# Optimization experiments

Hardware: AMD Instinct MI355X
Metric: run time of the kernel (lower is better)

The kernel has to match this reference:

```python
import jax, jax.numpy as jnp
import numpy as np

B, L, C = 64, 64, 16          # batch, seq_len, chars per word
V, CV = 100000, 100           # word vocab, char vocab
EMB, CHD = 300, 64            # word emb dim, char emb dim
N_HIGHWAY, N_ATTN = 2, 2
D = EMB + 3 * 50              # highway_dim = 450


def setup_inputs() -> dict:
    ks = jax.random.split(jax.random.key(0), 16)
    word_emb = jax.random.normal(ks[6], (V, EMB), jnp.float32) * 0.01
    word_emb = word_emb.at[0].set(0.0)  # padding_idx row zeroed
    return {
        "q1": jax.random.randint(ks[0], (B, L), 0, V),
        "q2": jax.random.randint(ks[1], (B, L), 0, V),
        "q1_len": jax.random.randint(ks[2], (B,), 1, L + 1),
        "q2_len": jax.random.randint(ks[3], (B,), 1, L + 1),
        "q1_char": jax.random.randint(ks[4], (B, L, C), 0, CV),
        "q2_char": jax.random.randint(ks[5], (B, L, C), 0, CV),
        "word_emb": word_emb,
        "char_emb": jax.random.normal(ks[7], (CV, CHD), jnp.float32) * 0.1,
        "conv_w3": jax.random.normal(ks[8], (50, CHD, 3), jnp.float32) / np.sqrt(CHD * 3),
        "conv_b3": jnp.zeros((50,), jnp.float32),
        "conv_w4": jax.random.normal(ks[9], (50, CHD, 4), jnp.float32) / np.sqrt(CHD * 4),
        "conv_b4": jnp.zeros((50,), jnp.float32),
        "conv_w5": jax.random.normal(ks[10], (50, CHD, 5), jnp.float32) / np.sqrt(CHD * 5),
        "conv_b5": jnp.zeros((50,), jnp.float32),
        "hw_w": jax.random.normal(ks[11], (D, D), jnp.float32) / np.sqrt(D),
        "hw_b": jnp.zeros((D,), jnp.float32),
        "attn_w": jax.random.normal(ks[12], (N_ATTN, 3 * D), jnp.float32) / np.sqrt(3 * D),
        "attn_b": jnp.zeros((N_ATTN,), jnp.float32),
    }


def _char_features(qc, emb, convs):
    # qc: [B, T, C] int -> [B, T, 150]
    Bq, T, Cc = qc.shape
    e = emb[qc.reshape(-1, Cc)].transpose(0, 2, 1)  # [B*T, CHD, C]
    outs = []
    for w, b in convs:
        h = jax.lax.conv_general_dilated(e, w, (1,), 'VALID',
                                         dimension_numbers=('NCH', 'OIH', 'NCH'))
        h = jax.nn.relu(h + b[None, :, None])
        outs.append(jnp.max(h, axis=2))  # max over char positions
    return jnp.concatenate(outs, axis=-1).reshape(Bq, T, -1)


def _highway(x, w, b):
    # NB: original reuses the SAME linear for transform and gate (bug-faithful)
    y = x @ w.T + b
    g = jax.nn.sigmoid(y)
    return g * jax.nn.relu(y) + (1.0 - g) * x


def _self_attn(x, mask, w, b):
    # Exact decomposition of Linear(concat(x_i, x_j, x_i*x_j)) -> scalar:
    # score[b,i,j] = x_i.w1 + x_j.w2 + sum_d x_i x_j w3 + b
    d = x.shape[-1]
    w1, w2, w3 = w[:d], w[d:2 * d], w[2 * d:]
    scores = ((x @ w1)[:, :, None] + (x @ w2)[:, None, :]
              + jnp.einsum('bid,bjd->bij', x * w3, x) + b)
    # original masked_fill uses -1e-09 (not -1e9) -- reproduce faithfully
    logits = jnp.where(mask[:, None, :], scores, jnp.float32(-1e-9))
    attn = jax.nn.softmax(logits, axis=-1)
    return jnp.einsum('bij,bjd->bid', attn, x)


def _branch(q, q_char, q_len, word_emb, char_emb, convs, hw_w, hw_b, attn_w, attn_b):
    mask = jnp.arange(L)[None, :] < q_len[:, None]
    x = jnp.concatenate([word_emb[q], _char_features(q_char, char_emb, convs)], axis=-1)
    for _ in range(N_HIGHWAY):
        x = _highway(x, hw_w, hw_b)
    att = x
    for i in range(N_ATTN):
        att = _self_attn(x, mask, attn_w[i], attn_b[i])
        x = att + x
    return att


def reference(q1, q2, q1_len, q2_len, q1_char, q2_char, word_emb, char_emb,
              conv_w3, conv_b3, conv_w4, conv_b4, conv_w5, conv_b5,
              hw_w, hw_b, attn_w, attn_b):
    convs = [(conv_w3, conv_b3), (conv_w4, conv_b4), (conv_w5, conv_b5)]
    a1 = _branch(q1, q1_char, q1_len, word_emb, char_emb, convs, hw_w, hw_b, attn_w, attn_b)
    a2 = _branch(q2, q2_char, q2_len, word_emb, char_emb, convs, hw_w, hw_b, attn_w, attn_b)
    return (a1, a2)
```

## Files before the change

### kernel.cpp

```cpp
#include <hip/hip_runtime.h>
#include <math.h>

#define B   64
#define L   64
#define C   16
#define CHD 64
#define EMB 300
#define D   450
#define DP  480
#define NT  (B*L)
#define NBH 128

typedef short bf16x8 __attribute__((ext_vector_type(8)));
typedef float f32x4  __attribute__((ext_vector_type(4)));
typedef float f32x2  __attribute__((ext_vector_type(2)));
typedef unsigned short ushort_t;
typedef ushort_t us4 __attribute__((ext_vector_type(4)));

#define MFMA16 __builtin_amdgcn_mfma_f32_16x16x32_bf16

#define WPF_N (10 * 10 * 512)
#define WBF_N (32 * 15 * 512)
#define XFRAG 30720

#define XFS 456
#define XSS 488

__device__ inline float wave_sum(float v) {
#pragma unroll
    for (int o = 32; o; o >>= 1) v += __shfl_xor(v, o, 64);
    return v;
}
__device__ inline ushort_t f2b(float f) {
    union { float f; unsigned u; } c; c.f = f;
    unsigned r = c.u + 0x7FFFu + ((c.u >> 16) & 1u);
    return (ushort_t)(r >> 16);
}

__global__ __launch_bounds__(256) void prep_kernel(
    const float* __restrict__ W,
    const float* __restrict__ w3, const float* __restrict__ b3,
    const float* __restrict__ w4, const float* __restrict__ b4,
    const float* __restrict__ w5, const float* __restrict__ b5,
    const float* __restrict__ char_emb,
    ushort_t* __restrict__ Wb16F, ushort_t* __restrict__ WpadF,
    float* __restrict__ bias160, ushort_t* __restrict__ ceb16)
{
    int idx = blockIdx.x * 256 + threadIdx.x;
    if (idx < WBF_N) {
        const int e = idx & 7, l = (idx >> 3) & 63, t = idx >> 9;
        const int ks = t % 15, nt = t / 15;
        const int ln = l & 15, q = l >> 4;
        const int n = nt * 16 + ln, k = ks * 32 + q * 8 + e;
        float v = (n < D && k < D) ? W[(size_t)n * D + k] : 0.f;
        Wb16F[idx] = f2b(v);
        return;
    }
    idx -= WBF_N;
    if (idx < WPF_N) {
        const int e = idx & 7, l = (idx >> 3) & 63, t = idx >> 9;
        const int ks = t % 10, nt = t / 10;
        const int ln = l & 15, q = l >> 4;
        const int f = nt * 16 + ln;
        const int kd = ks * 32 + q * 8 + e;
        const int k = kd >> 6, d = kd & 63;
        float v = 0.f;
        if (f < 50)       { if (k < 3) v = w3[f * 192 + d * 3 + k]; }
        else if (f < 100) { if (k < 4) v = w4[(f - 50) * 256 + d * 4 + k]; }
        else if (f < 150) { v = w5[(f - 100) * 320 + d * 5 + k]; }
        WpadF[idx] = f2b(v);
        return;
    }
    idx -= WPF_N;
    if (idx < 160) {
        bias160[idx] = (idx < 50) ? b3[idx] : (idx < 100) ? b4[idx - 50]
                     : (idx < 150) ? b5[idx - 100] : 0.f;
    } else if (idx < 160 + 100 * 64) {
        int i = idx - 160;
        ceb16[i] = f2b(char_emb[i]);
    }
}

#define ESS 72
#define EST (20 * ESS)

__global__ __launch_bounds__(256) void embed_conv_kernel(
    const int* __restrict__ q1, const int* __restrict__ q2,
    const int* __restrict__ q1c, const int* __restrict__ q2c,
    const float* __restrict__ word_emb, const ushort_t* __restrict__ ceb16,
    const ushort_t* __restrict__ WpadF, const float* __restrict__ bias160,
    float* __restrict__ xout, ushort_t* __restrict__ xbF)
{
    __shared__ ushort_t es[8 * EST];
    __shared__ ushort_t Xt[8 * XSS];

    const int tid  = threadIdx.x;
    const int wv   = tid >> 6;
    const int lane = tid & 63;
    const int ln   = lane & 15, quad = lane >> 4;
    const int bx   = blockIdx.x;
    const int tokbase = ((bx & 7) * 128 + (bx >> 3)) * 8;

#pragma unroll
    for (int i = 0; i < 4; ++i) {
        int c = tid + i * 256;
        int row = c >> 3, part = c & 7;
        int tl = row >> 4, cr = row & 15;
        int gtok   = tokbase + tl;
        int branch = gtok >> 12;
        int tokl   = gtok & (NT - 1);
        int cid    = (branch ? q2c : q1c)[tokl * C + cr];
        *(bf16x8*)&es[tl * EST + cr * ESS + part * 8] =
            *(const bf16x8*)&ceb16[cid * 64 + part * 8];
    }
    {
        int tl = tid >> 5, rr = (tid >> 3) & 3, part = tid & 7;
        bf16x8 z = {0, 0, 0, 0, 0, 0, 0, 0};
        *(bf16x8*)&es[tl * EST + (16 + rr) * ESS + part * 8] = z;
    }

#pragma unroll 1
    for (int c = tid; c < 8 * 75; c += 256) {
        const int t  = c / 75, d4 = c - t * 75;
        const int tok    = tokbase + t;
        const int branch = tok >> 12;
        const int tokl   = tok & (NT - 1);
        const int w      = (branch ? q2 : q1)[tokl];
        const float4 v = *(const float4*)(word_emb + (size_t)w * EMB + d4 * 4);
        float* dst = xout + (size_t)tok * D + d4 * 4;
        *(f32x2*)dst       = (f32x2){v.x, v.y};
        *(f32x2*)(dst + 2) = (f32x2){v.z, v.w};
        us4 pk = { f2b(v.x), f2b(v.y), f2b(v.z), f2b(v.w) };
        *(us4*)&Xt[t * XSS + d4 * 4] = pk;
    }
    if (tid < 240) {
        const int t = tid / 30, k = tid - t * 30;
        Xt[t * XSS + D + k] = 0;
    }
    __syncthreads();

    const int t0 = wv * 2, t1 = t0 + 1;
    f32x4 acc[2][10];
#pragma unroll
    for (int t = 0; t < 2; ++t)
#pragma unroll
        for (int nt = 0; nt < 10; ++nt) acc[t][nt] = (f32x4){0.f, 0.f, 0.f, 0.f};

#pragma unroll 1
    for (int ks = 0; ks < 10; ++ks) {
        const int kk   = ks * 32 + quad * 8;
        const int arow = kk >> 6, aoff = kk & 63;
        bf16x8 a0 = *(const bf16x8*)&es[t0 * EST + (ln + arow) * ESS + aoff];
        bf16x8 a1 = *(const bf16x8*)&es[t1 * EST + (ln + arow) * ESS + aoff];
#pragma unroll
        for (int nt = 0; nt < 10; ++nt) {
            bf16x8 bf = *(const bf16x8*)&WpadF[(size_t)((nt * 10 + ks) << 9) + lane * 8];
            acc[0][nt] = MFMA16(a0, bf, acc[0][nt], 0, 0, 0);
            acc[1][nt] = MFMA16(a1, bf, acc[1][nt], 0, 0, 0);
        }
    }
    __syncthreads();

    float* smf = (float*)es;
#pragma unroll
    for (int t = 0; t < 2; ++t) {
        const int tloc = t0 + t;
#pragma unroll
        for (int nt = 0; nt < 10; ++nt) {
            const int f  = nt * 16 + ln;
            const int Pf = (f < 50) ? 14 : (f < 100) ? 13 : 12;
            float m = -1e30f;
#pragma unroll
            for (int r = 0; r < 4; ++r) {
                const int p = quad * 4 + r;
                if (p < Pf) m = fmaxf(m, acc[t][nt][r]);
            }
            m = fmaxf(m, __shfl_xor(m, 16, 64));
            m = fmaxf(m, __shfl_xor(m, 32, 64));
            if (quad == 0) smf[tloc * 160 + f] = fmaxf(0.f, m + bias160[f]);
        }
    }
    __syncthreads();
#pragma unroll 1
    for (int c = tid; c < 8 * 150; c += 256) {
        const int t = c / 150, f = c - t * 150;
        const float rv = smf[t * 160 + f];
        xout[(size_t)(tokbase + t) * D + EMB + f] = rv;
        Xt[t * XSS + EMB + f] = f2b(rv);
    }
    __syncthreads();

    {
        const int tile = tokbase >> 4, half = (tokbase >> 3) & 1;
#pragma unroll 1
        for (int c = tid; c < 480; c += 256) {
            const int ksl = c >> 5, s = c & 31;
            const int q = s >> 3, tl = s & 7;
            const int l = q * 16 + half * 8 + tl;
            bf16x8 v = *(const bf16x8*)&Xt[tl * XSS + ksl * 32 + q * 8];
            *(bf16x8*)&xbF[((size_t)(tile * 15 + ksl) * 64 + l) * 8] = v;
        }
    }
}

#define HLS 72

__global__ __launch_bounds__(256, 4) void highway_mfma_kernel(
    const ushort_t* __restrict__ xbFi, const float* __restrict__ xf32,
    const ushort_t* __restrict__ Wb16F, const float* __restrict__ bvec,
    float* __restrict__ out, ushort_t* __restrict__ xbFo)
{
    __shared__ ushort_t Xl[64 * HLS];

    const int bx = blockIdx.x;
    const int cx = bx & 7, rr = bx >> 3;
    const int my = cx * 16 + (rr & 15);
    const int mx = rr >> 4;

    const int tid  = threadIdx.x;
    const int wv   = tid >> 6;
    const int lane = tid & 63;
    const int wm = wv >> 1, wn = wv & 1;
    const int m0 = my * 64 + wm * 32;
    const int n0 = mx * 64 + wn * 32;
    const int lm = lane & 15, quad = lane >> 4;

    const int tA0 = my * 4 + wm * 2;
    const ushort_t* ax0 = xbFi + (size_t)(tA0 * 15) * 512 + lane * 8;
    const ushort_t* ax1 = ax0 + 15 * 512;
    const int ntg0 = mx * 4 + wn * 2;
    const ushort_t* bw0 = Wb16F + (size_t)(ntg0 * 15) * 512 + lane * 8;
    const ushort_t* bw1 = bw0 + 15 * 512;

    f32x4 acc[2][2];
#pragma unroll
    for (int i = 0; i < 2; ++i)
#pragma unroll
        for (int j = 0; j < 2; ++j) acc[i][j] = (f32x4){0.f, 0.f, 0.f, 0.f};

#pragma unroll 3
    for (int ks = 0; ks < 15; ++ks) {
        bf16x8 a0 = *(const bf16x8*)(ax0 + ks * 512);
        bf16x8 a1 = *(const bf16x8*)(ax1 + ks * 512);
        bf16x8 b0 = *(const bf16x8*)(bw0 + ks * 512);
        bf16x8 b1 = *(const bf16x8*)(bw1 + ks * 512);
        acc[0][0] = MFMA16(a0, b0, acc[0][0], 0, 0, 0);
        acc[0][1] = MFMA16(a0, b1, acc[0][1], 0, 0, 0);
        acc[1][0] = MFMA16(a1, b0, acc[1][0], 0, 0, 0);
        acc[1][1] = MFMA16(a1, b1, acc[1][1], 0, 0, 0);
    }

#pragma unroll
    for (int nt = 0; nt < 2; ++nt) {
        const int n  = n0 + nt * 16 + lm;
        const int nl = wn * 32 + nt * 16 + lm;
        const bool nval = (n < D);
        const float bv = nval ? bvec[n] : 0.f;
#pragma unroll
        for (int mt = 0; mt < 2; ++mt) {
#pragma unroll
            for (int r = 0; r < 4; ++r) {
                const int m  = m0 + mt * 16 + quad * 4 + r;
                const int ml = wm * 32 + mt * 16 + quad * 4 + r;
                float y = acc[mt][nt][r] + bv;
                float g = 1.f / (1.f + __expf(-y));
                float o = 0.f;
                if (nval) {
                    float xo = xf32[(size_t)m * D + n];
                    o = g * fmaxf(y, 0.f) + (1.f - g) * xo;
                    out[(size_t)m * D + n] = o;
                }
                Xl[ml * HLS + nl] = f2b(nval ? o : 0.f);
            }
        }
    }
    __syncthreads();

#pragma unroll 1
    for (int c = tid; c < 512; c += 256) {
        const int fi = c >> 6, l = c & 63;
        const int tl = fi >> 1, ksl = fi & 1;
        const int ksg = mx * 2 + ksl;
        if (ksg < 15) {
            const int lnp = l & 15, qp = l >> 4;
            bf16x8 v = *(const bf16x8*)&Xl[(tl * 16 + lnp) * HLS + ksl * 32 + qp * 8];
            *(bf16x8*)&xbFo[((size_t)((my * 4 + tl) * 15 + ksg) * 64 + l) * 8] = v;
        }
    }
}

__global__ __launch_bounds__(512, 4) void highway2_prep_kernel(
    const ushort_t* __restrict__ xbFi, const float* __restrict__ xf32in,
    const ushort_t* __restrict__ Wb16F, const float* __restrict__ bvec,
    const float* __restrict__ attn_w,
    float* __restrict__ outf, ushort_t* __restrict__ xbFo,
    ushort_t* __restrict__ xw3F, ushort_t* __restrict__ xTF,
    float* __restrict__ s1g, float* __restrict__ s2g)
{
    __shared__ float Xf[16 * XFS];

    const int bx  = blockIdx.x;
    const int wid = (bx & 7) * 64 + (bx >> 3);
    const int bh  = wid >> 2, jq = wid & 3;
    const int tt  = wid;
    const int m0  = tt * 16;
    const int tid = threadIdx.x;
    const int wv  = tid >> 6;
    const int lane = tid & 63;
    const int ln = lane & 15, quad = lane >> 4;

    const ushort_t* ax = xbFi + (size_t)(tt * 15) * 512 + lane * 8;
    f32x4 acc[4];
#pragma unroll
    for (int t = 0; t < 4; ++t) acc[t] = (f32x4){0.f, 0.f, 0.f, 0.f};

#pragma unroll 1
    for (int ks = 0; ks < 15; ++ks) {
        bf16x8 a = *(const bf16x8*)(ax + ks * 512);
#pragma unroll
        for (int t = 0; t < 4; ++t) {
            const int nt = wv * 4 + t;
            if (nt < 30) {
                bf16x8 b = *(const bf16x8*)&Wb16F[(size_t)(nt * 15 + ks) * 512 + lane * 8];
                acc[t] = MFMA16(a, b, acc[t], 0, 0, 0);
            }
        }
    }

#pragma unroll
    for (int t = 0; t < 4; ++t) {
        const int nt = wv * 4 + t;
        if (nt >= 30) continue;
        const int n = nt * 16 + ln;
        const bool nval = (n < D);
        const float bv = nval ? bvec[n] : 0.f;
#pragma unroll
        for (int reg = 0; reg < 4; ++reg) {
            const int i = quad * 4 + reg;
            float y = acc[t][reg] + bv;
            float g = 1.f / (1.f + __expf(-y));
            if (nval) {
                float xo = xf32in[(size_t)(m0 + i) * D + n];
                float o = g * fmaxf(y, 0.f) + (1.f - g) * xo;
                outf[(size_t)(m0 + i) * D + n] = o;
                Xf[i * XFS + n] = o;
            }
        }
    }
    __syncthreads();

    const float* wb = attn_w;
    const float* w3 = wb + 2 * D;

#pragma unroll 1
    for (int rr = 0; rr < 2; ++rr) {
        const int j = wv * 2 + rr;
        float a1 = 0.f, a2 = 0.f;
#pragma unroll
        for (int t = 0; t < 8; ++t) {
            const int k = lane + t * 64;
            if (k < D) {
                float xv = Xf[j * XFS + k];
                a1 = fmaf(xv, wb[k], a1);
                a2 = fmaf(xv, wb[D + k], a2);
            }
        }
        a1 = wave_sum(a1);
        a2 = wave_sum(a2);
        if (lane == 0) { s1g[m0 + j] = a1; s2g[m0 + j] = a2; }
    }

#pragma unroll 1
    for (int c = tid; c < 960; c += 512) {
        const int ks = c >> 6, l = c & 63;
        const int lnp = l & 15, qp = l >> 4;
        bf16x8 v, pv;
#pragma unroll
        for (int e = 0; e < 8; ++e) {
            const int k = ks * 32 + qp * 8 + e;
            const float x = (k < D) ? Xf[lnp * XFS + k] : 0.f;
            v[e]  = (short)((k < D) ? f2b(x) : 0);
            pv[e] = (short)f2b((k < D) ? x * w3[k] : 0.f);
        }
        *(bf16x8*)&xbFo[((size_t)(tt * 15 + ks) * 64 + l) * 8] = v;
        *(bf16x8*)&xw3F[(size_t)bh * XFRAG + ((jq * 15 + ks) * 64 + l) * 8] = pv;
    }

    {
        const int half = jq >> 1, q0 = (jq & 1) * 2;
#pragma unroll 1
        for (int c = tid; c < 960; c += 512) {
            const int dt = c >> 5, s = c & 31;
            const int qp = q0 + (s >> 4), lnp = s & 15;
            const int d  = dt * 16 + lnp;
            const int jb = (qp & 1) * 8;
            bf16x8 v;
#pragma unroll
            for (int e = 0; e < 8; ++e)
                v[e] = (short)((d < D) ? f2b(Xf[(jb + e) * XFS + d]) : 0);
            *(bf16x8*)&xTF[(size_t)bh * XFRAG + ((dt * 2 + half) * 64 + qp * 16 + lnp) * 8] = v;
        }
    }
}

#define ALS 72

__global__ __launch_bounds__(512, 4) void attn_core_prep_kernel(
    const float* __restrict__ xf32,
    const ushort_t* __restrict__ xF, const ushort_t* __restrict__ xw3F,
    const ushort_t* __restrict__ xTF,
    const float* __restrict__ s1g, const float* __restrict__ s2g,
    const int* __restrict__ q1_len, const int* __restrict__ q2_len,
    const float* __restrict__ attn_b, const float* __restrict__ attn_w,
    ushort_t* __restrict__ xbFo,
    ushort_t* __restrict__ xw3Fo, ushort_t* __restrict__ xTFo,
    float* __restrict__ s1o, float* __restrict__ s2o)
{
    __shared__ float    sc[16][68];
    __shared__ ushort_t Al[16 * ALS];
    __shared__ float    Qp[4 * 256];
    __shared__ float    Af[16 * XFS];

    const int bx  = blockIdx.x;
    const int wid = (bx & 7) * 64 + (bx >> 3);
    const int bh  = wid >> 2, iq = wid & 3;
    const int branch = bh >> 6, b = bh & 63;
    const int tid  = threadIdx.x;
    const int wv   = tid >> 6;
    const int lane = tid & 63;
    const int ln   = lane & 15, quad = lane >> 4;
    const int i0   = iq * 16;
    const int m0   = bh * 64 + i0;
    const int jt   = wv & 3, hks = wv >> 2;

    const ushort_t* xa = xF   + (size_t)bh * XFRAG + (iq * 15 * 64 + lane) * 8;
    const ushort_t* xb = xw3F + (size_t)bh * XFRAG + (jt * 15 * 64 + lane) * 8;

    f32x4 qa = (f32x4){0.f, 0.f, 0.f, 0.f};
    if (hks == 0) {
#pragma unroll
        for (int ks = 0; ks < 15; ks += 2) {
            bf16x8 a  = *(const bf16x8*)(xa + ks * 512);
            bf16x8 bq = *(const bf16x8*)(xb + ks * 512);
            qa = MFMA16(a, bq, qa, 0, 0, 0);
        }
    } else {
#pragma unroll
        for (int ks = 1; ks < 15; ks += 2) {
            bf16x8 a  = *(const bf16x8*)(xa + ks * 512);
            bf16x8 bq = *(const bf16x8*)(xb + ks * 512);
            qa = MFMA16(a, bq, qa, 0, 0, 0);
        }
        *(f32x4*)&Qp[jt * 256 + lane * 4] = qa;
    }
    __syncthreads();

    const int   len  = (branch ? q2_len : q1_len)[b];
    if (hks == 0) {
        f32x4 qo = *(const f32x4*)&Qp[jt * 256 + lane * 4];
        f32x4 qacc = qa + qo;
        const float bias = attn_b[0];
        const int   j    = jt * 16 + ln;
        const float s2v  = s2g[bh * 64 + j];
#pragma unroll
        for (int reg = 0; reg < 4; ++reg) {
            const int i = i0 + quad * 4 + reg;
            float v = qacc[reg] + s1g[bh * 64 + i] + s2v + bias;
            if (j >= len) v = -1e-9f;
            sc[quad * 4 + reg][j] = v;
        }
    }
    __syncthreads();

#pragma unroll
    for (int rr = 0; rr < 2; ++rr) {
        const int r = wv * 2 + rr;
        float v = sc[r][lane];
        float m = v;
#pragma unroll
        for (int o = 32; o; o >>= 1) m = fmaxf(m, __shfl_xor(m, o, 64));
        float ev = __expf(v - m);
        float sm = ev;
#pragma unroll
        for (int o = 32; o; o >>= 1) sm += __shfl_xor(sm, o, 64);
        Al[r * ALS + lane] = f2b(ev * (1.f / sm));
    }
    __syncthreads();

    const ushort_t* xTb = xTF + (size_t)bh * XFRAG + lane * 8;
    bf16x8 af0 = *(const bf16x8*)&Al[ln * ALS + quad * 8];
    bf16x8 af1 = *(const bf16x8*)&Al[ln * ALS + quad * 8 + 32];

#pragma unroll 2
    for (int dt = wv; dt < 30; dt += 8) {
        bf16x8 b0 = *(const bf16x8*)(xTb + dt * 1024);
        bf16x8 b1 = *(const bf16x8*)(xTb + dt * 1024 + 512);
        f32x4 acc = (f32x4){0.f, 0.f, 0.f, 0.f};
        acc = MFMA16(af0, b0, acc, 0, 0, 0);
        acc = MFMA16(af1, b1, acc, 0, 0, 0);

        const int d = dt * 16 + ln;
        if (d < D) {
#pragma unroll
            for (int reg = 0; reg < 4; ++reg) {
                const int il = quad * 4 + reg;
                float v = acc[reg] + xf32[(size_t)(m0 + il) * D + d];
                Af[il * XFS + d] = v;
            }
        }
    }
    __syncthreads();

    const float* wb1 = attn_w + 3 * D;
    const float* w31 = wb1 + 2 * D;

#pragma unroll 1
    for (int rr = 0; rr < 2; ++rr) {
        const int jj = wv * 2 + rr;
        float a1 = 0.f, a2 = 0.f;
#pragma unroll
        for (int t = 0; t < 8; ++t) {
            const int k = lane + t * 64;
            if (k < D) {
                float xv = Af[jj * XFS + k];
                a1 = fmaf(xv, wb1[k], a1);
                a2 = fmaf(xv, wb1[D + k], a2);
            }
        }
        a1 = wave_sum(a1);
        a2 = wave_sum(a2);
        if (lane == 0) { s1o[m0 + jj] = a1; s2o[m0 + jj] = a2; }
    }

#pragma unroll 1
    for (int c = tid; c < 960; c += 512) {
        const int ks = c >> 6, l = c & 63;
        const int lnp = l & 15, qp = l >> 4;
        bf16x8 v, pv;
#pragma unroll
        for (int e = 0; e < 8; ++e) {
            const int k = ks * 32 + qp * 8 + e;
            const float x = (k < D) ? Af[lnp * XFS + k] : 0.f;
            v[e]  = (short)((k < D) ? f2b(x) : 0);
            pv[e] = (short)f2b((k < D) ? x * w31[k] : 0.f);
        }
        *(bf16x8*)&xbFo[((size_t)((bh * 4 + iq) * 15 + ks) * 64 + l) * 8] = v;
        *(bf16x8*)&xw3Fo[(size_t)bh * XFRAG + ((iq * 15 + ks) * 64 + l) * 8] = pv;
    }

    {
        const int half = iq >> 1, q0 = (iq & 1) * 2;
#pragma unroll 1
        for (int c = tid; c < 960; c += 512) {
            const int dt = c >> 5, s = c & 31;
            const int qp = q0 + (s >> 4), lnp = s & 15;
            const int d  = dt * 16 + lnp;
            const int jb = (qp & 1) * 8;
            bf16x8 v;
#pragma unroll
            for (int e = 0; e < 8; ++e)
                v[e] = (short)((d < D) ? f2b(Af[(jb + e) * XFS + d]) : 0);
            *(bf16x8*)&xTFo[(size_t)bh * XFRAG + ((dt * 2 + half) * 64 + qp * 16 + lnp) * 8] = v;
        }
    }
}

__global__ __launch_bounds__(512, 4) void attn_core_final_kernel(
    const ushort_t* __restrict__ xF, const ushort_t* __restrict__ xw3F,
    const ushort_t* __restrict__ xTF,
    const float* __restrict__ s1g, const float* __restrict__ s2g,
    const int* __restrict__ q1_len, const int* __restrict__ q2_len,
    const float* __restrict__ attn_b,
    float* __restrict__ outf)
{
    __shared__ float    sc[16][68];
    __shared__ ushort_t Al[16 * ALS];
    __shared__ float    Qp[4 * 256];

    const int bx  = blockIdx.x;
    const int wid = (bx & 7) * 64 + (bx >> 3);
    const int bh  = wid >> 2, iq = wid & 3;
    const int branch = bh >> 6, b = bh & 63;
    const int tid  = threadIdx.x;
    const int wv   = tid >> 6;
    const int lane = tid & 63;
    const int ln   = lane & 15, quad = lane >> 4;
    const int i0   = iq * 16;
    const int jt   = wv & 3, hks = wv >> 2;

    const ushort_t* xa = xF   + (size_t)bh * XFRAG + (iq * 15 * 64 + lane) * 8;
    const ushort_t* xb = xw3F + (size_t)bh * XFRAG + (jt * 15 * 64 + lane) * 8;

    f32x4 qa = (f32x4){0.f, 0.f, 0.f, 0.f};
    if (hks == 0) {
#pragma unroll
        for (int ks = 0; ks < 15; ks += 2) {
            bf16x8 a  = *(const bf16x8*)(xa + ks * 512);
            bf16x8 bq = *(const bf16x8*)(xb + ks * 512);
            qa = MFMA16(a, bq, qa, 0, 0, 0);
        }
    } else {
#pragma unroll
        for (int ks = 1; ks < 15; ks += 2) {
            bf16x8 a  = *(const bf16x8*)(xa + ks * 512);
            bf16x8 bq = *(const bf16x8*)(xb + ks * 512);
            qa = MFMA16(a, bq, qa, 0, 0, 0);
        }
        *(f32x4*)&Qp[jt * 256 + lane * 4] = qa;
    }
    __syncthreads();

    const int len = (branch ? q2_len : q1_len)[b];
    if (hks == 0) {
        f32x4 qo = *(const f32x4*)&Qp[jt * 256 + lane * 4];
        f32x4 qacc = qa + qo;
        const float bias = attn_b[1];
        const int   j    = jt * 16 + ln;
        const float s2v  = s2g[bh * 64 + j];
#pragma unroll
        for (int reg = 0; reg < 4; ++reg) {
            const int i = i0 + quad * 4 + reg;
            float v = qacc[reg] + s1g[bh * 64 + i] + s2v + bias;
            if (j >= len) v = -1e-9f;
            sc[quad * 4 + reg][j] = v;
        }
    }
    __syncthreads();

#pragma unroll
    for (int rr = 0; rr < 2; ++rr) {
        const int r = wv * 2 + rr;
        float v = sc[r][lane];
        float m = v;
#pragma unroll
        for (int o = 32; o; o >>= 1) m = fmaxf(m, __shfl_xor(m, o, 64));
        float ev = __expf(v - m);
        float sm = ev;
#pragma unroll
        for (int o = 32; o; o >>= 1) sm += __shfl_xor(sm, o, 64);
        Al[r * ALS + lane] = f2b(ev * (1.f / sm));
    }
    __syncthreads();

    const ushort_t* xTb = xTF + (size_t)bh * XFRAG + lane * 8;
    bf16x8 af0 = *(const bf16x8*)&Al[ln * ALS + quad * 8];
    bf16x8 af1 = *(const bf16x8*)&Al[ln * ALS + quad * 8 + 32];

#pragma unroll 2
    for (int dt = wv; dt < 30; dt += 8) {
        bf16x8 b0 = *(const bf16x8*)(xTb + dt * 1024);
        bf16x8 b1 = *(const bf16x8*)(xTb + dt * 1024 + 512);
        f32x4 acc = (f32x4){0.f, 0.f, 0.f, 0.f};
        acc = MFMA16(af0, b0, acc, 0, 0, 0);
        acc = MFMA16(af1, b1, acc, 0, 0, 0);

        const int d = dt * 16 + ln;
        if (d < D) {
#pragma unroll
            for (int reg = 0; reg < 4; ++reg) {
                const int i = i0 + quad * 4 + reg;
                outf[((size_t)bh * 64 + i) * D + d] = acc[reg];
            }
        }
    }
}

extern "C" void kernel_launch(void* const* d_in, const int* in_sizes, int n_in,
                              void* d_out, int out_size, void* d_ws, size_t ws_size,
                              hipStream_t stream) {
    const int*   q1       = (const int*)  d_in[0];
    const int*   q2       = (const int*)  d_in[1];
    const int*   q1_len   = (const int*)  d_in[2];
    const int*   q2_len   = (const int*)  d_in[3];
    const int*   q1c      = (const int*)  d_in[4];
    const int*   q2c      = (const int*)  d_in[5];
    const float* word_emb = (const float*)d_in[6];
    const float* char_emb = (const float*)d_in[7];
    const float* w3       = (const float*)d_in[8];
    const float* b3       = (const float*)d_in[9];
    const float* w4       = (const float*)d_in[10];
    const float* b4       = (const float*)d_in[11];
    const float* w5       = (const float*)d_in[12];
    const float* b5       = (const float*)d_in[13];
    const float* hw_w     = (const float*)d_in[14];
    const float* hw_b     = (const float*)d_in[15];
    const float* attn_w   = (const float*)d_in[16];
    const float* attn_b   = (const float*)d_in[17];
    float* out = (float*)d_out;

    float*    buf0    = (float*)d_ws;
    float*    buf1    = buf0 + (size_t)2 * NT * D;
    float*    bias160 = buf1 + (size_t)2 * NT * D;
    ushort_t* xbFa    = (ushort_t*)(bias160 + 160);
    ushort_t* xbFb    = xbFa + (size_t)2 * NT * DP;
    ushort_t* Wb16F   = xbFb + (size_t)2 * NT * DP;
    ushort_t* WpadF   = Wb16F + (size_t)WBF_N;
    ushort_t* ceb16   = WpadF + (size_t)WPF_N;
    ushort_t* xw3Fa   = ceb16 + (size_t)100 * 64;
    ushort_t* xTFa    = xw3Fa + (size_t)NBH * XFRAG;
    ushort_t* xw3Fb   = xTFa  + (size_t)NBH * XFRAG;
    ushort_t* xTFb    = xw3Fb + (size_t)NBH * XFRAG;
    float*    s1a     = (float*)(xTFb + (size_t)NBH * XFRAG);
    float*    s2a     = s1a + (size_t)2 * NT;
    float*    s1b     = s2a + (size_t)2 * NT;
    float*    s2b     = s1b + (size_t)2 * NT;

    prep_kernel<<<(WBF_N + WPF_N + 160 + 100 * 64 + 255) / 256, 256, 0, stream>>>(
        hw_w, w3, b3, w4, b4, w5, b5, char_emb, Wb16F, WpadF, bias160, ceb16);
    embed_conv_kernel<<<1024, 256, 0, stream>>>(q1, q2, q1c, q2c, word_emb, ceb16,
                                                WpadF, bias160, buf0, xbFa);

    highway_mfma_kernel<<<1024, 256, 0, stream>>>(xbFa, buf0, Wb16F, hw_b, buf1, xbFb);

    highway2_prep_kernel<<<512, 512, 0, stream>>>(
        xbFb, buf1, Wb16F, hw_b, attn_w, buf0, xbFa, xw3Fa, xTFa, s1a, s2a);

    attn_core_prep_kernel<<<512, 512, 0, stream>>>(
        buf0, xbFa, xw3Fa, xTFa, s1a, s2a, q1_len, q2_len, attn_b, attn_w,
        xbFb, xw3Fb, xTFb, s1b, s2b);

    attn_core_final_kernel<<<512, 512, 0, stream>>>(
        xbFb, xw3Fb, xTFb, s1b, s2b, q1_len, q2_len, attn_b, out);
}
```

Measured before the change: 306.0 us.

## Fuse embedding, char conv and both highway layers into one front kernel

Merges the embed+char-conv kernel, the first highway kernel and the second highway/attention-prep kernel into a single megafront kernel. Each block handles 16 tokens and keeps the activations in fp32 shared memory across stages, converting to bf16 on the fly for the MFMA A operand. This removes two launches and the global round-trips of intermediate fp32 and bf16-fragment buffers. The cost is that each block now streams the whole highway weight matrix twice, with scalar LDS reads and conversions to build A fragments, and uses more shared memory, which may lower occupancy.

```diff
diff --git a/kernel.cpp b/kernel.cpp
--- a/kernel.cpp
+++ b/kernel.cpp
@@ -13,9 +13,7 @@
 
 typedef short bf16x8 __attribute__((ext_vector_type(8)));
 typedef float f32x4  __attribute__((ext_vector_type(4)));
-typedef float f32x2  __attribute__((ext_vector_type(2)));
 typedef unsigned short ushort_t;
-typedef ushort_t us4 __attribute__((ext_vector_type(4)));
 
 #define MFMA16 __builtin_amdgcn_mfma_f32_16x16x32_bf16
 
@@ -23,8 +21,7 @@
 #define WBF_N (32 * 15 * 512)
 #define XFRAG 30720
 
-#define XFS 456
-#define XSS 488
+#define XFS 457
 
 __device__ inline float wave_sum(float v) {
 #pragma unroll
@@ -84,220 +81,19 @@
 #define ESS 72
 #define EST (20 * ESS)
 
-__global__ __launch_bounds__(256) void embed_conv_kernel(
+__global__ __launch_bounds__(512, 4) void megafront_kernel(
     const int* __restrict__ q1, const int* __restrict__ q2,
     const int* __restrict__ q1c, const int* __restrict__ q2c,
     const float* __restrict__ word_emb, const ushort_t* __restrict__ ceb16,
     const ushort_t* __restrict__ WpadF, const float* __restrict__ bias160,
-    float* __restrict__ xout, ushort_t* __restrict__ xbF)
-{
-    __shared__ ushort_t es[8 * EST];
-    __shared__ ushort_t Xt[8 * XSS];
-
-    const int tid  = threadIdx.x;
-    const int wv   = tid >> 6;
-    const int lane = tid & 63;
-    const int ln   = lane & 15, quad = lane >> 4;
-    const int bx   = blockIdx.x;
-    const int tokbase = ((bx & 7) * 128 + (bx >> 3)) * 8;
-
-#pragma unroll
-    for (int i = 0; i < 4; ++i) {
-        int c = tid + i * 256;
-        int row = c >> 3, part = c & 7;
-        int tl = row >> 4, cr = row & 15;
-        int gtok   = tokbase + tl;
-        int branch = gtok >> 12;
-        int tokl   = gtok & (NT - 1);
-        int cid    = (branch ? q2c : q1c)[tokl * C + cr];
-        *(bf16x8*)&es[tl * EST + cr * ESS + part * 8] =
-            *(const bf16x8*)&ceb16[cid * 64 + part * 8];
-    }
-    {
-        int tl = tid >> 5, rr = (tid >> 3) & 3, part = tid & 7;
-        bf16x8 z = {0, 0, 0, 0, 0, 0, 0, 0};
-        *(bf16x8*)&es[tl * EST + (16 + rr) * ESS + part * 8] = z;
-    }
-
-#pragma unroll 1
-    for (int c = tid; c < 8 * 75; c += 256) {
-        const int t  = c / 75, d4 = c - t * 75;
-        const int tok    = tokbase + t;
-        const int branch = tok >> 12;
-        const int tokl   = tok & (NT - 1);
-        const int w      = (branch ? q2 : q1)[tokl];
-        const float4 v = *(const float4*)(word_emb + (size_t)w * EMB + d4 * 4);
-        float* dst = xout + (size_t)tok * D + d4 * 4;
-        *(f32x2*)dst       = (f32x2){v.x, v.y};
-        *(f32x2*)(dst + 2) = (f32x2){v.z, v.w};
-        us4 pk = { f2b(v.x), f2b(v.y), f2b(v.z), f2b(v.w) };
-        *(us4*)&Xt[t * XSS + d4 * 4] = pk;
-    }
-    if (tid < 240) {
-        const int t = tid / 30, k = tid - t * 30;
-        Xt[t * XSS + D + k] = 0;
-    }
-    __syncthreads();
-
-    const int t0 = wv * 2, t1 = t0 + 1;
-    f32x4 acc[2][10];
-#pragma unroll
-    for (int t = 0; t < 2; ++t)
-#pragma unroll
-        for (int nt = 0; nt < 10; ++nt) acc[t][nt] = (f32x4){0.f, 0.f, 0.f, 0.f};
-
-#pragma unroll 1
-    for (int ks = 0; ks < 10; ++ks) {
-        const int kk   = ks * 32 + quad * 8;
-        const int arow = kk >> 6, aoff = kk & 63;
-        bf16x8 a0 = *(const bf16x8*)&es[t0 * EST + (ln + arow) * ESS + aoff];
-        bf16x8 a1 = *(const bf16x8*)&es[t1 * EST + (ln + arow) * ESS + aoff];
-#pragma unroll
-        for (int nt = 0; nt < 10; ++nt) {
-            bf16x8 bf = *(const bf16x8*)&WpadF[(size_t)((nt * 10 + ks) << 9) + lane * 8];
-            acc[0][nt] = MFMA16(a0, bf, acc[0][nt], 0, 0, 0);
-            acc[1][nt] = MFMA16(a1, bf, acc[1][nt], 0, 0, 0);
-        }
-    }
-    __syncthreads();
-
-    float* smf = (float*)es;
-#pragma unroll
-    for (int t = 0; t < 2; ++t) {
-        const int tloc = t0 + t;
-#pragma unroll
-        for (int nt = 0; nt < 10; ++nt) {
-            const int f  = nt * 16 + ln;
-            const int Pf = (f < 50) ? 14 : (f < 100) ? 13 : 12;
-            float m = -1e30f;
-#pragma unroll
-            for (int r = 0; r < 4; ++r) {
-                const int p = quad * 4 + r;
-                if (p < Pf) m = fmaxf(m, acc[t][nt][r]);
-            }
-            m = fmaxf(m, __shfl_xor(m, 16, 64));
-            m = fmaxf(m, __shfl_xor(m, 32, 64));
-            if (quad == 0) smf[tloc * 160 + f] = fmaxf(0.f, m + bias160[f]);
-        }
-    }
-    __syncthreads();
-#pragma unroll 1
-    for (int c = tid; c < 8 * 150; c += 256) {
-        const int t = c / 150, f = c - t * 150;
-        const float rv = smf[t * 160 + f];
-        xout[(size_t)(tokbase + t) * D + EMB + f] = rv;
-        Xt[t * XSS + EMB + f] = f2b(rv);
-    }
-    __syncthreads();
-
-    {
-        const int tile = tokbase >> 4, half = (tokbase >> 3) & 1;
-#pragma unroll 1
-        for (int c = tid; c < 480; c += 256) {
-            const int ksl = c >> 5, s = c & 31;
-            const int q = s >> 3, tl = s & 7;
-            const int l = q * 16 + half * 8 + tl;
-            bf16x8 v = *(const bf16x8*)&Xt[tl * XSS + ksl * 32 + q * 8];
-            *(bf16x8*)&xbF[((size_t)(tile * 15 + ksl) * 64 + l) * 8] = v;
-        }
-    }
-}
-
-#define HLS 72
-
-__global__ __launch_bounds__(256, 4) void highway_mfma_kernel(
-    const ushort_t* __restrict__ xbFi, const float* __restrict__ xf32,
-    const ushort_t* __restrict__ Wb16F, const float* __restrict__ bvec,
-    float* __restrict__ out, ushort_t* __restrict__ xbFo)
-{
-    __shared__ ushort_t Xl[64 * HLS];
-
-    const int bx = blockIdx.x;
-    const int cx = bx & 7, rr = bx >> 3;
-    const int my = cx * 16 + (rr & 15);
-    const int mx = rr >> 4;
-
-    const int tid  = threadIdx.x;
-    const int wv   = tid >> 6;
-    const int lane = tid & 63;
-    const int wm = wv >> 1, wn = wv & 1;
-    const int m0 = my * 64 + wm * 32;
-    const int n0 = mx * 64 + wn * 32;
-    const int lm = lane & 15, quad = lane >> 4;
-
-    const int tA0 = my * 4 + wm * 2;
-    const ushort_t* ax0 = xbFi + (size_t)(tA0 * 15) * 512 + lane * 8;
-    const ushort_t* ax1 = ax0 + 15 * 512;
-    const int ntg0 = mx * 4 + wn * 2;
-    const ushort_t* bw0 = Wb16F + (size_t)(ntg0 * 15) * 512 + lane * 8;
-    const ushort_t* bw1 = bw0 + 15 * 512;
-
-    f32x4 acc[2][2];
-#pragma unroll
-    for (int i = 0; i < 2; ++i)
-#pragma unroll
-        for (int j = 0; j < 2; ++j) acc[i][j] = (f32x4){0.f, 0.f, 0.f, 0.f};
-
-#pragma unroll 3
-    for (int ks = 0; ks < 15; ++ks) {
-        bf16x8 a0 = *(const bf16x8*)(ax0 + ks * 512);
-        bf16x8 a1 = *(const bf16x8*)(ax1 + ks * 512);
-        bf16x8 b0 = *(const bf16x8*)(bw0 + ks * 512);
-        bf16x8 b1 = *(const bf16x8*)(bw1 + ks * 512);
-        acc[0][0] = MFMA16(a0, b0, acc[0][0], 0, 0, 0);
-        acc[0][1] = MFMA16(a0, b1, acc[0][1], 0, 0, 0);
-        acc[1][0] = MFMA16(a1, b0, acc[1][0], 0, 0, 0);
-        acc[1][1] = MFMA16(a1, b1, acc[1][1], 0, 0, 0);
-    }
-
-#pragma unroll
-    for (int nt = 0; nt < 2; ++nt) {
-        const int n  = n0 + nt * 16 + lm;
-        const int nl = wn * 32 + nt * 16 + lm;
-        const bool nval = (n < D);
-        const float bv = nval ? bvec[n] : 0.f;
-#pragma unroll
-        for (int mt = 0; mt < 2; ++mt) {
-#pragma unroll
-            for (int r = 0; r < 4; ++r) {
-                const int m  = m0 + mt * 16 + quad * 4 + r;
-                const int ml = wm * 32 + mt * 16 + quad * 4 + r;
-                float y = acc[mt][nt][r] + bv;
-                float g = 1.f / (1.f + __expf(-y));
-                float o = 0.f;
-                if (nval) {
-                    float xo = xf32[(size_t)m * D + n];
-                    o = g * fmaxf(y, 0.f) + (1.f - g) * xo;
-                    out[(size_t)m * D + n] = o;
-                }
-                Xl[ml * HLS + nl] = f2b(nval ? o : 0.f);
-            }
-        }
-    }
-    __syncthreads();
-
-#pragma unroll 1
-    for (int c = tid; c < 512; c += 256) {
-        const int fi = c >> 6, l = c & 63;
-        const int tl = fi >> 1, ksl = fi & 1;
-        const int ksg = mx * 2 + ksl;
-        if (ksg < 15) {
-            const int lnp = l & 15, qp = l >> 4;
-            bf16x8 v = *(const bf16x8*)&Xl[(tl * 16 + lnp) * HLS + ksl * 32 + qp * 8];
-            *(bf16x8*)&xbFo[((size_t)((my * 4 + tl) * 15 + ksg) * 64 + l) * 8] = v;
-        }
-    }
-}
-
-__global__ __launch_bounds__(512, 4) void highway2_prep_kernel(
-    const ushort_t* __restrict__ xbFi, const float* __restrict__ xf32in,
-    const ushort_t* __restrict__ Wb16F, const float* __restrict__ bvec,
+    const ushort_t* __restrict__ Wb16F, const float* __restrict__ hw_b,
     const float* __restrict__ attn_w,
     float* __restrict__ outf, ushort_t* __restrict__ xbFo,
     ushort_t* __restrict__ xw3F, ushort_t* __restrict__ xTF,
     float* __restrict__ s1g, float* __restrict__ s2g)
 {
-    __shared__ float Xf[16 * XFS];
+    __shared__ ushort_t es[16 * EST];
+    __shared__ float    Xf[16 * XFS];
 
     const int bx  = blockIdx.x;
     const int wid = (bx & 7) * 64 + (bx >> 3);
@@ -309,45 +105,134 @@
     const int lane = tid & 63;
     const int ln = lane & 15, quad = lane >> 4;
 
-    const ushort_t* ax = xbFi + (size_t)(tt * 15) * 512 + lane * 8;
-    f32x4 acc[4];
-#pragma unroll
-    for (int t = 0; t < 4; ++t) acc[t] = (f32x4){0.f, 0.f, 0.f, 0.f};
-
-#pragma unroll 1
-    for (int ks = 0; ks < 15; ++ks) {
-        bf16x8 a = *(const bf16x8*)(ax + ks * 512);
+#pragma unroll
+    for (int i = 0; i < 4; ++i) {
+        int c = tid + i * 512;
+        int row = c >> 3, part = c & 7;
+        int tl = row >> 4, cr = row & 15;
+        int gtok   = m0 + tl;
+        int branch = gtok >> 12;
+        int tokl   = gtok & (NT - 1);
+        int cid    = (branch ? q2c : q1c)[tokl * C + cr];
+        *(bf16x8*)&es[tl * EST + cr * ESS + part * 8] =
+            *(const bf16x8*)&ceb16[cid * 64 + part * 8];
+    }
+    {
+        int tl = tid >> 5, rr = (tid >> 3) & 3, part = tid & 7;
+        bf16x8 z = {0, 0, 0, 0, 0, 0, 0, 0};
+        *(bf16x8*)&es[tl * EST + (16 + rr) * ESS + part * 8] = z;
+    }
+
+#pragma unroll 1
+    for (int c = tid; c < 16 * 75; c += 512) {
+        const int t  = c / 75, d4 = c - t * 75;
+        const int gtok   = m0 + t;
+        const int branch = gtok >> 12;
+        const int tokl   = gtok & (NT - 1);
+        const int w      = (branch ? q2 : q1)[tokl];
+        const float4 v = *(const float4*)(word_emb + (size_t)w * EMB + d4 * 4);
+        float* dst = &Xf[t * XFS + d4 * 4];
+        dst[0] = v.x; dst[1] = v.y; dst[2] = v.z; dst[3] = v.w;
+    }
+    __syncthreads();
+
+    {
+        const int t0 = wv * 2, t1 = t0 + 1;
+        f32x4 acc[2][10];
+#pragma unroll
+        for (int t = 0; t < 2; ++t)
+#pragma unroll
+            for (int nt = 0; nt < 10; ++nt) acc[t][nt] = (f32x4){0.f, 0.f, 0.f, 0.f};
+
+#pragma unroll 1
+        for (int ks = 0; ks < 10; ++ks) {
+            const int kk   = ks * 32 + quad * 8;
+            const int arow = kk >> 6, aoff = kk & 63;
+            bf16x8 a0 = *(const bf16x8*)&es[t0 * EST + (ln + arow) * ESS + aoff];
+            bf16x8 a1 = *(const bf16x8*)&es[t1 * EST + (ln + arow) * ESS + aoff];
+#pragma unroll
+            for (int nt = 0; nt < 10; ++nt) {
+                bf16x8 bf = *(const bf16x8*)&WpadF[(size_t)((nt * 10 + ks) << 9) + lane * 8];
+                acc[0][nt] = MFMA16(a0, bf, acc[0][nt], 0, 0, 0);
+                acc[1][nt] = MFMA16(a1, bf, acc[1][nt], 0, 0, 0);
+            }
+        }
+        __syncthreads();
+
+        float* smf = (float*)es;
+#pragma unroll
+        for (int t = 0; t < 2; ++t) {
+            const int tloc = t0 + t;
+#pragma unroll
+            for (int nt = 0; nt < 10; ++nt) {
+                const int f  = nt * 16 + ln;
+                const int Pf = (f < 50) ? 14 : (f < 100) ? 13 : 12;
+                float m = -1e30f;
+#pragma unroll
+                for (int r = 0; r < 4; ++r) {
+                    const int p = quad * 4 + r;
+                    if (p < Pf) m = fmaxf(m, acc[t][nt][r]);
+                }
+                m = fmaxf(m, __shfl_xor(m, 16, 64));
+                m = fmaxf(m, __shfl_xor(m, 32, 64));
+                if (quad == 0) smf[tloc * 160 + f] = fmaxf(0.f, m + bias160[f]);
+            }
+        }
+        __syncthreads();
+#pragma unroll 1
+        for (int c = tid; c < 16 * 150; c += 512) {
+            const int t = c / 150, f = c - t * 150;
+            Xf[t * XFS + EMB + f] = smf[t * 160 + f];
+        }
+    }
+    __syncthreads();
+
+#pragma unroll 1
+    for (int h = 0; h < 2; ++h) {
+        f32x4 hacc[4];
+#pragma unroll
+        for (int t = 0; t < 4; ++t) hacc[t] = (f32x4){0.f, 0.f, 0.f, 0.f};
+
+#pragma unroll 1
+        for (int ks = 0; ks < 15; ++ks) {
+            bf16x8 a;
+#pragma unroll
+            for (int e = 0; e < 8; ++e) {
+                const int k = ks * 32 + quad * 8 + e;
+                a[e] = (short)((k < D) ? f2b(Xf[ln * XFS + k]) : 0);
+            }
+#pragma unroll
+            for (int t = 0; t < 4; ++t) {
+                const int nt = wv * 4 + t;
+                if (nt < 30) {
+                    bf16x8 b = *(const bf16x8*)&Wb16F[(size_t)(nt * 15 + ks) * 512 + lane * 8];
+                    hacc[t] = MFMA16(a, b, hacc[t], 0, 0, 0);
+                }
+            }
+        }
+        __syncthreads();
+
 #pragma unroll
         for (int t = 0; t < 4; ++t) {
             const int nt = wv * 4 + t;
-            if (nt < 30) {
-                bf16x8 b = *(const bf16x8*)&Wb16F[(size_t)(nt * 15 + ks) * 512 + lane * 8];
-                acc[t] = MFMA16(a, b, acc[t], 0, 0, 0);
-            }
-        }
-    }
-
-#pragma unroll
-    for (int t = 0; t < 4; ++t) {
-        const int nt = wv * 4 + t;
-        if (nt >= 30) continue;
-        const int n = nt * 16 + ln;
-        const bool nval = (n < D);
-        const float bv = nval ? bvec[n] : 0.f;
-#pragma unroll
-        for (int reg = 0; reg < 4; ++reg) {
-            const int i = quad * 4 + reg;
-            float y = acc[t][reg] + bv;
-            float g = 1.f / (1.f + __expf(-y));
-            if (nval) {
-                float xo = xf32in[(size_t)(m0 + i) * D + n];
-                float o = g * fmaxf(y, 0.f) + (1.f - g) * xo;
-                outf[(size_t)(m0 + i) * D + n] = o;
-                Xf[i * XFS + n] = o;
-            }
-        }
-    }
-    __syncthreads();
+            if (nt >= 30) continue;
+            const int n = nt * 16 + ln;
+            if (n < D) {
+                const float bv = hw_b[n];
+#pragma unroll
+                for (int reg = 0; reg < 4; ++reg) {
+                    const int i = quad * 4 + reg;
+                    float y = hacc[t][reg] + bv;
+                    float g = 1.f / (1.f + __expf(-y));
+                    float xo = Xf[i * XFS + n];
+                    float o = g * fmaxf(y, 0.f) + (1.f - g) * xo;
+                    Xf[i * XFS + n] = o;
+                    if (h == 1) outf[(size_t)(m0 + i) * D + n] = o;
+                }
+            }
+        }
+        __syncthreads();
+    }
 
     const float* wb = attn_w;
     const float* w3 = wb + 2 * D;
@@ -707,13 +592,10 @@
 
     prep_kernel<<<(WBF_N + WPF_N + 160 + 100 * 64 + 255) / 256, 256, 0, stream>>>(
         hw_w, w3, b3, w4, b4, w5, b5, char_emb, Wb16F, WpadF, bias160, ceb16);
-    embed_conv_kernel<<<1024, 256, 0, stream>>>(q1, q2, q1c, q2c, word_emb, ceb16,
-                                                WpadF, bias160, buf0, xbFa);
-
-    highway_mfma_kernel<<<1024, 256, 0, stream>>>(xbFa, buf0, Wb16F, hw_b, buf1, xbFb);
-
-    highway2_prep_kernel<<<512, 512, 0, stream>>>(
-        xbFb, buf1, Wb16F, hw_b, attn_w, buf0, xbFa, xw3Fa, xTFa, s1a, s2a);
+
+    megafront_kernel<<<512, 512, 0, stream>>>(
+        q1, q2, q1c, q2c, word_emb, ceb16, WpadF, bias160, Wb16F, hw_b,
+        attn_w, buf0, xbFa, xw3Fa, xTFa, s1a, s2a);
 
     attn_core_prep_kernel<<<512, 512, 0, stream>>>(
         buf0, xbFa, xw3Fa, xTFa, s1a, s2a, q1_len, q2_len, attn_b, attn_w,
```

After: 283.5 us. -7.3%, faster.
